# Optimization experiments

Hardware: AMD Instinct MI355X
Metric: run time of the kernel (lower is better)

Reference implementation:

```python
import jax, jax.numpy as jnp
import numpy as np

N = 100000
E = 625000
D_IN = 128
D_OUT = 128
EPS = 0.0  # GINConv default eps, non-trainable


def setup_inputs() -> dict:
    key = jax.random.key(0)
    k1, k2, k3 = jax.random.split(key, 3)
    x = jax.random.normal(k1, (N, D_IN), dtype=jnp.float32)
    edge_index = jax.random.randint(k2, (2, E), 0, N, dtype=jnp.int64)
    # torch Linear weight [out, in], bias [out]
    W = jax.random.normal(k3, (D_OUT, D_IN), dtype=jnp.float32) / np.sqrt(D_IN)
    b = jnp.zeros((D_OUT,), dtype=jnp.float32)
    return {"x": x, "edge_index": edge_index, "W": W, "b": b}


def reference(x, edge_index, W, b):
    src, dst = edge_index[0], edge_index[1]
    # message = x[src], sum-aggregated at dst (GIN sum aggregation)
    agg = jax.ops.segment_sum(x[src], dst, num_segments=N)  # [N, D_IN]
    h = (1.0 + EPS) * x + agg
    # MLP: Linear then ReLU
    out = jax.nn.relu(jnp.einsum("nd,od->no", h, W) + b)  # [N, D_OUT]
    return out
```

## Files before the change

kernel.cpp:

```cpp
#include <hip/hip_runtime.h>
#include <hip/hip_bf16.h>

#define N_NODES 100000
#define E_EDGES 625000
#define D 128

#define CAP 32
#define T1_CNT 0
#define T1_BKT 100352
#define T1_INTS (T1_BKT + N_NODES * CAP)

#define OFF_OFS 0
#define CUR_OFS 100004
#define BKT_OFS (CUR_OFS + N_NODES)
#define BSM_OFS (BKT_OFS + E_EDGES)
#define WS_INTS (BSM_OFS + 64)

#define SCAN_CHUNK 2048
#define SCAN_BLOCKS ((N_NODES + SCAN_CHUNK - 1) / SCAN_CHUNK)

typedef short s16x8 __attribute__((ext_vector_type(8)));
typedef unsigned short us8 __attribute__((ext_vector_type(8)));
typedef unsigned short us4 __attribute__((ext_vector_type(4)));
typedef float f32x4 __attribute__((ext_vector_type(4)));

static __device__ __forceinline__ unsigned short f2bf(float f) {
    unsigned int u = __builtin_bit_cast(unsigned int, f);
    u += 0x7fffu + ((u >> 16) & 1u);
    return (unsigned short)(u >> 16);
}

__global__ void fill_direct(const int* __restrict__ ei, int* cnt,
                            int* __restrict__ bucket) {
    int e = blockIdx.x * 256 + threadIdx.x;
    if (e < E_EDGES) {
        int dst = ei[E_EDGES + e];
        int pos = atomicAdd(&cnt[dst], 1);
        if (pos < CAP) bucket[(size_t)dst * CAP + pos] = ei[e];
    }
}

#define BM2 128
__global__ __launch_bounds__(512) void fused_gather_gemm_v2(
        const float* __restrict__ x, const int* __restrict__ cnt,
        const int* __restrict__ bucket, const float* __restrict__ W,
        const float* __restrict__ bias, float* __restrict__ out, int n) {
    __shared__ unsigned short hA[BM2 * D];
    __shared__ unsigned short wB[D * D];
    const int tid = threadIdx.x;
    const int row0 = blockIdx.x * BM2;

    for (int c = tid; c < D * D / 8; c += 512) {
        int r = c >> 4, ch = c & 15;
        const float4* p = (const float4*)&W[(size_t)r * D + ch * 8];
        float4 p0 = p[0], p1 = p[1];
        us8 o;
        o[0] = f2bf(p0.x); o[1] = f2bf(p0.y); o[2] = f2bf(p0.z); o[3] = f2bf(p0.w);
        o[4] = f2bf(p1.x); o[5] = f2bf(p1.y); o[6] = f2bf(p1.z); o[7] = f2bf(p1.w);
        unsigned int byte = (unsigned)(r * 256 + ch * 16) ^ ((r & 15) << 4);
        *(us8*)&wB[byte >> 1] = o;
    }

    const int hw = tid >> 5, q = tid & 31;
    const float4* x4 = (const float4*)x;
#pragma unroll
    for (int i = 0; i < 8; ++i) {
        int r = i * 16 + hw;
        int grow = row0 + r;
        float ax = 0.f, ay = 0.f, az = 0.f, aw = 0.f;
        if (grow < n) {
            float4 self = x4[(size_t)grow * 32 + q];
            ax = self.x; ay = self.y; az = self.z; aw = self.w;
            int deg = cnt[grow]; if (deg > CAP) deg = CAP;
            const int* bk = bucket + (size_t)grow * CAP;
            float bx = 0.f, by = 0.f, bz = 0.f, bw = 0.f;
            float cx = 0.f, cy = 0.f, cz = 0.f, cw = 0.f;
            float dx = 0.f, dy = 0.f, dz = 0.f, dw = 0.f;
            int j = 0;
            for (; j + 3 < deg; j += 4) {
                int s0 = bk[j], s1 = bk[j + 1], s2 = bk[j + 2], s3 = bk[j + 3];
                float4 v0 = x4[(size_t)s0 * 32 + q];
                float4 v1 = x4[(size_t)s1 * 32 + q];
                float4 v2 = x4[(size_t)s2 * 32 + q];
                float4 v3 = x4[(size_t)s3 * 32 + q];
                ax += v0.x; ay += v0.y; az += v0.z; aw += v0.w;
                bx += v1.x; by += v1.y; bz += v1.z; bw += v1.w;
                cx += v2.x; cy += v2.y; cz += v2.z; cw += v2.w;
                dx += v3.x; dy += v3.y; dz += v3.z; dw += v3.w;
            }
            for (; j < deg; ++j) {
                int s0 = bk[j];
                float4 v0 = x4[(size_t)s0 * 32 + q];
                ax += v0.x; ay += v0.y; az += v0.z; aw += v0.w;
            }
            ax += bx + cx + dx; ay += by + cy + dy;
            az += bz + cz + dz; aw += bw + cw + dw;
        }
        us4 o;
        o[0] = f2bf(ax); o[1] = f2bf(ay); o[2] = f2bf(az); o[3] = f2bf(aw);
        unsigned int byte = (unsigned)(r * 256 + q * 8) ^ ((r & 15) << 4);
        *(us4*)&hA[byte >> 1] = o;
    }
    __syncthreads();

    const int w = tid >> 6, lane = tid & 63;
    const int wr = (w >> 1) * 32;
    const int wc = (w & 1) * 64;
    const int lr = lane & 15;
    const int kb = (lane >> 4) * 8;

    f32x4 acc[2][4] = {};
    for (int k0 = 0; k0 < D; k0 += 32) {
        s16x8 af[2], bfr[4];
#pragma unroll
        for (int m = 0; m < 2; ++m) {
            int r = wr + m * 16 + lr;
            unsigned int byte = (unsigned)(r * 256 + (k0 + kb) * 2) ^ ((r & 15) << 4);
            af[m] = *(s16x8*)&hA[byte >> 1];
        }
#pragma unroll
        for (int nn = 0; nn < 4; ++nn) {
            int o = wc + nn * 16 + lr;
            unsigned int byte = (unsigned)(o * 256 + (k0 + kb) * 2) ^ ((o & 15) << 4);
            bfr[nn] = *(s16x8*)&wB[byte >> 1];
        }
#pragma unroll
        for (int m = 0; m < 2; ++m)
#pragma unroll
            for (int nn = 0; nn < 4; ++nn)
                acc[m][nn] = __builtin_amdgcn_mfma_f32_16x16x32_bf16(af[m], bfr[nn],
                                                                     acc[m][nn], 0, 0, 0);
    }

    const int cr4 = (lane >> 4) * 4;
#pragma unroll
    for (int m = 0; m < 2; ++m) {
#pragma unroll
        for (int r = 0; r < 4; ++r) {
            int grow = row0 + wr + m * 16 + cr4 + r;
            if (grow < n) {
#pragma unroll
                for (int nn = 0; nn < 4; ++nn) {
                    int col = wc + nn * 16 + (lane & 15);
                    float v = acc[m][nn][r] + bias[col];
                    out[(size_t)grow * D + col] = fmaxf(v, 0.0f);
                }
            }
        }
    }
}

__global__ void hist_kernel(const int* __restrict__ ei, int* cnt) {
    int e = blockIdx.x * 256 + threadIdx.x;
    if (e < E_EDGES) atomicAdd(&cnt[ei[E_EDGES + e]], 1);
}

__global__ __launch_bounds__(256) void scan_partial(const int* __restrict__ cnt,
                                                    int* __restrict__ bsum) {
    __shared__ int wsum[4];
    const int b = blockIdx.x, t = threadIdx.x;
    const int base = b * SCAN_CHUNK + t * 8;
    int s = 0;
#pragma unroll
    for (int k = 0; k < 8; ++k) {
        int i = base + k;
        if (i < N_NODES) s += cnt[i];
    }
    for (int d = 32; d > 0; d >>= 1) s += __shfl_xor(s, d);
    if ((t & 63) == 0) wsum[t >> 6] = s;
    __syncthreads();
    if (t == 0) bsum[b] = wsum[0] + wsum[1] + wsum[2] + wsum[3];
}

__global__ void scan_bsums(int* bsum, int* off) {
    int t = threadIdx.x;
    int orig = (t < SCAN_BLOCKS) ? bsum[t] : 0;
    int v = orig;
    for (int d = 1; d < 64; d <<= 1) {
        int u = __shfl_up(v, d);
        if (t >= d) v += u;
    }
    if (t < SCAN_BLOCKS) bsum[t] = v - orig;
    if (t == 0) off[N_NODES] = E_EDGES;
}

__global__ __launch_bounds__(256) void scan_final(const int* __restrict__ cnt,
                                                  const int* __restrict__ bsum,
                                                  int* __restrict__ off,
                                                  int* __restrict__ cur) {
    __shared__ int woff[4];
    const int b = blockIdx.x, t = threadIdx.x;
    const int w = t >> 6, lane = t & 63;
    const int base = b * SCAN_CHUNK + t * 8;
    int v[8];
    int s = 0;
#pragma unroll
    for (int k = 0; k < 8; ++k) {
        int i = base + k;
        v[k] = (i < N_NODES) ? cnt[i] : 0;
        s += v[k];
    }
    int inc = s;
    for (int d = 1; d < 64; d <<= 1) {
        int u = __shfl_up(inc, d);
        if (lane >= d) inc += u;
    }
    if (lane == 63) woff[w] = inc;
    __syncthreads();
    if (t == 0) {
        int run = 0;
        for (int i = 0; i < 4; ++i) { int xx = woff[i]; woff[i] = run; run += xx; }
    }
    __syncthreads();
    int prefix = bsum[b] + woff[w] + (inc - s);
#pragma unroll
    for (int k = 0; k < 8; ++k) {
        int i = base + k;
        if (i < N_NODES) { off[i] = prefix; cur[i] = prefix; prefix += v[k]; }
    }
}

__global__ void fill_kernel(const int* __restrict__ ei, int* cur, int* __restrict__ bucket) {
    int e = blockIdx.x * 256 + threadIdx.x;
    if (e < E_EDGES) {
        int dst = ei[E_EDGES + e];
        int pos = atomicAdd(&cur[dst], 1);
        bucket[pos] = ei[e];
    }
}

#define BM 64
__global__ __launch_bounds__(256) void fused_gather_gemm(
        const float* __restrict__ x, const int* __restrict__ off,
        const int* __restrict__ bucket, const float* __restrict__ W,
        const float* __restrict__ bias, float* __restrict__ out, int n) {
    __shared__ unsigned short hA[BM * D];
    __shared__ unsigned short wB[D * D];
    const int tid = threadIdx.x;
    const int row0 = blockIdx.x * BM;

    for (int c = tid; c < D * D / 8; c += 256) {
        int r = c >> 4, ch = c & 15;
        const float4* p = (const float4*)&W[(size_t)r * D + ch * 8];
        float4 p0 = p[0], p1 = p[1];
        us8 o;
        o[0] = f2bf(p0.x); o[1] = f2bf(p0.y); o[2] = f2bf(p0.z); o[3] = f2bf(p0.w);
        o[4] = f2bf(p1.x); o[5] = f2bf(p1.y); o[6] = f2bf(p1.z); o[7] = f2bf(p1.w);
        unsigned int byte = (unsigned)(r * 256 + ch * 16) ^ ((r & 15) << 4);
        *(us8*)&wB[byte >> 1] = o;
    }

    const int hw = tid >> 5, q = tid & 31;
    const float4* x4 = (const float4*)x;
#pragma unroll
    for (int i = 0; i < 8; ++i) {
        int r = i * 8 + hw;
        int grow = row0 + r;
        float ax = 0.f, ay = 0.f, az = 0.f, aw = 0.f;
        if (grow < n) {
            float4 self = x4[(size_t)grow * 32 + q];
            ax = self.x; ay = self.y; az = self.z; aw = self.w;
            int beg = off[grow], end = off[grow + 1];
            float bx = 0.f, by = 0.f, bz = 0.f, bw = 0.f;
            int j = beg;
            for (; j + 1 < end; j += 2) {
                int s0 = bucket[j], s1 = bucket[j + 1];
                float4 v0 = x4[(size_t)s0 * 32 + q];
                float4 v1 = x4[(size_t)s1 * 32 + q];
                ax += v0.x; ay += v0.y; az += v0.z; aw += v0.w;
                bx += v1.x; by += v1.y; bz += v1.z; bw += v1.w;
            }
            if (j < end) {
                int s0 = bucket[j];
                float4 v0 = x4[(size_t)s0 * 32 + q];
                ax += v0.x; ay += v0.y; az += v0.z; aw += v0.w;
            }
            ax += bx; ay += by; az += bz; aw += bw;
        }
        us4 o;
        o[0] = f2bf(ax); o[1] = f2bf(ay); o[2] = f2bf(az); o[3] = f2bf(aw);
        unsigned int byte = (unsigned)(r * 256 + q * 8) ^ ((r & 15) << 4);
        *(us4*)&hA[byte >> 1] = o;
    }
    __syncthreads();

    const int w = tid >> 6, lane = tid & 63;
    const int wr = (w >> 1) * 32;
    const int wc = (w & 1) * 64;
    const int lr = lane & 15;
    const int kb = (lane >> 4) * 8;

    f32x4 acc[2][4] = {};
    for (int k0 = 0; k0 < D; k0 += 32) {
        s16x8 af[2], bfr[4];
#pragma unroll
        for (int m = 0; m < 2; ++m) {
            int r = wr + m * 16 + lr;
            unsigned int byte = (unsigned)(r * 256 + (k0 + kb) * 2) ^ ((r & 15) << 4);
            af[m] = *(s16x8*)&hA[byte >> 1];
        }
#pragma unroll
        for (int nn = 0; nn < 4; ++nn) {
            int o = wc + nn * 16 + lr;
            unsigned int byte = (unsigned)(o * 256 + (k0 + kb) * 2) ^ ((o & 15) << 4);
            bfr[nn] = *(s16x8*)&wB[byte >> 1];
        }
#pragma unroll
        for (int m = 0; m < 2; ++m)
#pragma unroll
            for (int nn = 0; nn < 4; ++nn)
                acc[m][nn] = __builtin_amdgcn_mfma_f32_16x16x32_bf16(af[m], bfr[nn],
                                                                     acc[m][nn], 0, 0, 0);
    }

    const int cr4 = (lane >> 4) * 4;
#pragma unroll
    for (int m = 0; m < 2; ++m) {
#pragma unroll
        for (int r = 0; r < 4; ++r) {
            int grow = row0 + wr + m * 16 + cr4 + r;
            if (grow < n) {
#pragma unroll
                for (int nn = 0; nn < 4; ++nn) {
                    int col = wc + nn * 16 + (lane & 15);
                    float v = acc[m][nn][r] + bias[col];
                    out[(size_t)grow * D + col] = fmaxf(v, 0.0f);
                }
            }
        }
    }
}

__global__ void init_h(const float4* __restrict__ x, float4* __restrict__ h, int n4) {
    int g = blockIdx.x * 256 + threadIdx.x;
    if (g < n4) h[g] = x[g];
}

__global__ void scatter_add(const float* __restrict__ x, const int* __restrict__ ei,
                            float* __restrict__ h) {
    long long g = (long long)blockIdx.x * 256 + threadIdx.x;
    if (g >= (long long)E_EDGES * 32) return;
    int e = (int)(g >> 5);
    int q = (int)(g & 31);
    int src = ei[e];
    int dst = ei[E_EDGES + e];
    float4 v = *(const float4*)&x[(long long)src * D + q * 4];
    float* p = &h[(long long)dst * D + q * 4];
    atomicAdd(p + 0, v.x);
    atomicAdd(p + 1, v.y);
    atomicAdd(p + 2, v.z);
    atomicAdd(p + 3, v.w);
}

__global__ __launch_bounds__(256) void gemm_relu_mfma(const float* __restrict__ h_in,
                                                      const float* __restrict__ W,
                                                      const float* __restrict__ bias,
                                                      float* __restrict__ out, int n) {
    __shared__ unsigned short hA[BM * D];
    __shared__ unsigned short wB[D * D];
    const int tid = threadIdx.x;
    const int row0 = blockIdx.x * BM;

    for (int c = tid; c < BM * D / 8; c += 256) {
        int r = c >> 4, ch = c & 15;
        int grow = row0 + r;
        us8 o = {};
        if (grow < n) {
            const float4* p = (const float4*)&h_in[(size_t)grow * D + ch * 8];
            float4 p0 = p[0], p1 = p[1];
            o[0] = f2bf(p0.x); o[1] = f2bf(p0.y); o[2] = f2bf(p0.z); o[3] = f2bf(p0.w);
            o[4] = f2bf(p1.x); o[5] = f2bf(p1.y); o[6] = f2bf(p1.z); o[7] = f2bf(p1.w);
        }
        unsigned int byte = (unsigned)(r * 256 + ch * 16) ^ ((r & 15) << 4);
        *(us8*)&hA[byte >> 1] = o;
    }
    for (int c = tid; c < D * D / 8; c += 256) {
        int r = c >> 4, ch = c & 15;
        const float4* p = (const float4*)&W[(size_t)r * D + ch * 8];
        float4 p0 = p[0], p1 = p[1];
        us8 o;
        o[0] = f2bf(p0.x); o[1] = f2bf(p0.y); o[2] = f2bf(p0.z); o[3] = f2bf(p0.w);
        o[4] = f2bf(p1.x); o[5] = f2bf(p1.y); o[6] = f2bf(p1.z); o[7] = f2bf(p1.w);
        unsigned int byte = (unsigned)(r * 256 + ch * 16) ^ ((r & 15) << 4);
        *(us8*)&wB[byte >> 1] = o;
    }
    __syncthreads();

    const int w = tid >> 6, lane = tid & 63;
    const int wr = (w >> 1) * 32;
    const int wc = (w & 1) * 64;
    const int lr = lane & 15;
    const int kb = (lane >> 4) * 8;

    f32x4 acc[2][4] = {};
    for (int k0 = 0; k0 < D; k0 += 32) {
        s16x8 af[2], bfr[4];
#pragma unroll
        for (int m = 0; m < 2; ++m) {
            int r = wr + m * 16 + lr;
            unsigned int byte = (unsigned)(r * 256 + (k0 + kb) * 2) ^ ((r & 15) << 4);
            af[m] = *(s16x8*)&hA[byte >> 1];
        }
#pragma unroll
        for (int nn = 0; nn < 4; ++nn) {
            int o = wc + nn * 16 + lr;
            unsigned int byte = (unsigned)(o * 256 + (k0 + kb) * 2) ^ ((o & 15) << 4);
            bfr[nn] = *(s16x8*)&wB[byte >> 1];
        }
#pragma unroll
        for (int m = 0; m < 2; ++m)
#pragma unroll
            for (int nn = 0; nn < 4; ++nn)
                acc[m][nn] = __builtin_amdgcn_mfma_f32_16x16x32_bf16(af[m], bfr[nn],
                                                                     acc[m][nn], 0, 0, 0);
    }

    const int cr4 = (lane >> 4) * 4;
#pragma unroll
    for (int m = 0; m < 2; ++m) {
#pragma unroll
        for (int r = 0; r < 4; ++r) {
            int grow = row0 + wr + m * 16 + cr4 + r;
            if (grow < n) {
#pragma unroll
                for (int nn = 0; nn < 4; ++nn) {
                    int col = wc + nn * 16 + (lane & 15);
                    float v = acc[m][nn][r] + bias[col];
                    out[(size_t)grow * D + col] = fmaxf(v, 0.0f);
                }
            }
        }
    }
}

extern "C" void kernel_launch(void* const* d_in, const int* in_sizes, int n_in,
                              void* d_out, int out_size, void* d_ws, size_t ws_size,
                              hipStream_t stream) {
    const float* x  = (const float*)d_in[0];
    const int*   ei = (const int*)d_in[1];
    const float* W  = (const float*)d_in[2];
    const float* b  = (const float*)d_in[3];
    float* out = (float*)d_out;
    int eblocks = (E_EDGES + 255) / 256;

    if (ws_size >= (size_t)T1_INTS * sizeof(int)) {
        int* wsi = (int*)d_ws;
        hipMemsetAsync(wsi + T1_CNT, 0, N_NODES * sizeof(int), stream);
        fill_direct<<<eblocks, 256, 0, stream>>>(ei, wsi + T1_CNT, wsi + T1_BKT);
        int gblocks = (N_NODES + BM2 - 1) / BM2;
        fused_gather_gemm_v2<<<gblocks, 512, 0, stream>>>(x, wsi + T1_CNT, wsi + T1_BKT,
                                                          W, b, out, N_NODES);
    } else if (ws_size >= (size_t)WS_INTS * sizeof(int)) {
        int* wsi = (int*)d_ws;
        hipMemsetAsync(wsi + CUR_OFS, 0, N_NODES * sizeof(int), stream);
        hist_kernel<<<eblocks, 256, 0, stream>>>(ei, wsi + CUR_OFS);
        scan_partial<<<SCAN_BLOCKS, 256, 0, stream>>>(wsi + CUR_OFS, wsi + BSM_OFS);
        scan_bsums<<<1, 64, 0, stream>>>(wsi + BSM_OFS, wsi + OFF_OFS);
        scan_final<<<SCAN_BLOCKS, 256, 0, stream>>>(wsi + CUR_OFS, wsi + BSM_OFS,
                                                    wsi + OFF_OFS, wsi + CUR_OFS);
        fill_kernel<<<eblocks, 256, 0, stream>>>(ei, wsi + CUR_OFS, wsi + BKT_OFS);
        int mblocks = (N_NODES + BM - 1) / BM;
        fused_gather_gemm<<<mblocks, 256, 0, stream>>>(x, wsi + OFF_OFS, wsi + BKT_OFS,
                                                       W, b, out, N_NODES);
    } else {
        int n4 = N_NODES * D / 4;
        init_h<<<(n4 + 255) / 256, 256, 0, stream>>>((const float4*)x, (float4*)out, n4);
        long long sthreads = (long long)E_EDGES * 32;
        int sblocks = (int)((sthreads + 255) / 256);
        scatter_add<<<sblocks, 256, 0, stream>>>(x, ei, out);
        int mblocks = (N_NODES + BM - 1) / BM;
        gemm_relu_mfma<<<mblocks, 256, 0, stream>>>(out, W, b, out, N_NODES);
    }
}
```

Before: 195.0 us.

## Precompute bf16 weights once and shrink fused tile to raise occupancy

Adds a small kernel that converts W to bf16 into workspace once, so each block no longer converts and stages the full weight matrix in shared memory. The fused gather+GEMM now uses 64-row tiles with 256 threads and reads B fragments directly from global/L2. This cuts shared memory per block and should let more blocks reside per CU, helping hide gather latency. The trade-off is that B fragments are read from cache on every k-step instead of LDS, and there is one extra launch.

```diff
diff --git a/kernel.cpp b/kernel.cpp
--- a/kernel.cpp
+++ b/kernel.cpp
@@ -8,7 +8,8 @@
 #define CAP 32
 #define T1_CNT 0
 #define T1_BKT 100352
-#define T1_INTS (T1_BKT + N_NODES * CAP)
+#define T1_WBF (T1_BKT + N_NODES * CAP)
+#define T1_INTS (T1_WBF + D * D / 2 + 64)
 
 #define OFF_OFS 0
 #define CUR_OFS 100004
@@ -40,32 +41,32 @@
     }
 }
 
-#define BM2 128
-__global__ __launch_bounds__(512) void fused_gather_gemm_v2(
-        const float* __restrict__ x, const int* __restrict__ cnt,
-        const int* __restrict__ bucket, const float* __restrict__ W,
-        const float* __restrict__ bias, float* __restrict__ out, int n) {
-    __shared__ unsigned short hA[BM2 * D];
-    __shared__ unsigned short wB[D * D];
-    const int tid = threadIdx.x;
-    const int row0 = blockIdx.x * BM2;
-
-    for (int c = tid; c < D * D / 8; c += 512) {
-        int r = c >> 4, ch = c & 15;
-        const float4* p = (const float4*)&W[(size_t)r * D + ch * 8];
+__global__ void w_to_bf16(const float* __restrict__ W, unsigned short* __restrict__ wbf) {
+    int c = blockIdx.x * 256 + threadIdx.x;
+    if (c < D * D / 8) {
+        const float4* p = (const float4*)&W[c * 8];
         float4 p0 = p[0], p1 = p[1];
         us8 o;
         o[0] = f2bf(p0.x); o[1] = f2bf(p0.y); o[2] = f2bf(p0.z); o[3] = f2bf(p0.w);
         o[4] = f2bf(p1.x); o[5] = f2bf(p1.y); o[6] = f2bf(p1.z); o[7] = f2bf(p1.w);
-        unsigned int byte = (unsigned)(r * 256 + ch * 16) ^ ((r & 15) << 4);
-        *(us8*)&wB[byte >> 1] = o;
-    }
+        *(us8*)&wbf[c * 8] = o;
+    }
+}
+
+#define BM3 64
+__global__ __launch_bounds__(256) void fused_gather_gemm_v3(
+        const float* __restrict__ x, const int* __restrict__ cnt,
+        const int* __restrict__ bucket, const unsigned short* __restrict__ wbf,
+        const float* __restrict__ bias, float* __restrict__ out, int n) {
+    __shared__ unsigned short hA[BM3 * D];
+    const int tid = threadIdx.x;
+    const int row0 = blockIdx.x * BM3;
 
     const int hw = tid >> 5, q = tid & 31;
     const float4* x4 = (const float4*)x;
 #pragma unroll
     for (int i = 0; i < 8; ++i) {
-        int r = i * 16 + hw;
+        int r = i * 8 + hw;
         int grow = row0 + r;
         float ax = 0.f, ay = 0.f, az = 0.f, aw = 0.f;
         if (grow < n) {
@@ -121,8 +122,7 @@
 #pragma unroll
         for (int nn = 0; nn < 4; ++nn) {
             int o = wc + nn * 16 + lr;
-            unsigned int byte = (unsigned)(o * 256 + (k0 + kb) * 2) ^ ((o & 15) << 4);
-            bfr[nn] = *(s16x8*)&wB[byte >> 1];
+            bfr[nn] = *(const s16x8*)&wbf[(size_t)o * D + k0 + kb];
         }
 #pragma unroll
         for (int m = 0; m < 2; ++m)
@@ -446,10 +446,12 @@
     if (ws_size >= (size_t)T1_INTS * sizeof(int)) {
         int* wsi = (int*)d_ws;
         hipMemsetAsync(wsi + T1_CNT, 0, N_NODES * sizeof(int), stream);
+        w_to_bf16<<<(D * D / 8 + 255) / 256, 256, 0, stream>>>(W, (unsigned short*)(wsi + T1_WBF));
         fill_direct<<<eblocks, 256, 0, stream>>>(ei, wsi + T1_CNT, wsi + T1_BKT);
-        int gblocks = (N_NODES + BM2 - 1) / BM2;
-        fused_gather_gemm_v2<<<gblocks, 512, 0, stream>>>(x, wsi + T1_CNT, wsi + T1_BKT,
-                                                          W, b, out, N_NODES);
+        int gblocks = (N_NODES + BM3 - 1) / BM3;
+        fused_gather_gemm_v3<<<gblocks, 256, 0, stream>>>(
+            x, wsi + T1_CNT, wsi + T1_BKT, (const unsigned short*)(wsi + T1_WBF),
+            b, out, N_NODES);
     } else if (ws_size >= (size_t)WS_INTS * sizeof(int)) {
         int* wsi = (int*)d_ws;
         hipMemsetAsync(wsi + CUR_OFS, 0, N_NODES * sizeof(int), stream);
```

New measurement: 208.6 us. 7.0% more time.
